# Kernel tuning notes

Measured on AMD Instinct MI355X. Metric: run time of the kernel, lower is better.

The kernel has to match this reference:

```python
import jax, jax.numpy as jnp
import numpy as np

N = 100000          # num nodes
E = 1_600_000       # num edges (avg degree 16)
IN = 512
OUT = 64
HOPS = 4


def setup_inputs() -> dict:
    key = jax.random.key(0)
    k1, k2, k3 = jax.random.split(key, 3)
    x = jax.random.normal(k1, (N, IN), dtype=jnp.float32)
    W = jax.random.normal(k2, (OUT, IN), dtype=jnp.float32) * 0.02
    b = jnp.zeros((OUT,), dtype=jnp.float32)
    edge_index = jax.random.randint(k3, (2, E), 0, N, dtype=jnp.int32)
    return {"x": x, "W": W, "b": b, "edge_index": edge_index}


def reference(x, W, b, edge_index):
    # 1) linear projection first (low-memory SGC variant)
    h = x @ W.T + b                      # [N, OUT]
    n = h.shape[0]

    # 2) gcn_norm: add self loops, symmetric D^{-1/2} A D^{-1/2}
    row, col = edge_index[0], edge_index[1]
    loop = jnp.arange(n, dtype=row.dtype)
    row = jnp.concatenate([row, loop])   # [E+N]
    col = jnp.concatenate([col, loop])
    ew = jnp.ones(row.shape[0], dtype=h.dtype)
    deg = jax.ops.segment_sum(ew, col, num_segments=n)          # in-degree incl. self loop
    dinv = jnp.where(deg > 0, jax.lax.rsqrt(deg), 0.0)
    w = dinv[row] * ew * dinv[col]       # normalized edge weights [E+N]

    # 3) hops x SpMM: adj_t built with (row=col, col=row) => out[col] += w * h[row]
    for _ in range(HOPS):
        h = jax.ops.segment_sum(w[:, None] * h[row], col, num_segments=n)
    return h
```

## Files before the change

### kernel.cpp

```cpp
#include <hip/hip_runtime.h>
#include <stdint.h>

#define IN_DIM 512
#define OUT_DIM 64

typedef short bf16x8 __attribute__((ext_vector_type(8)));
typedef float f32x4 __attribute__((ext_vector_type(4)));

__device__ inline unsigned short f2bf(float f) {
    unsigned int u = __float_as_uint(f);
    return (unsigned short)((u + 0x7FFFu + ((u >> 16) & 1u)) >> 16);
}
__device__ inline float bf2f(unsigned short s) {
    return __uint_as_float(((unsigned int)s) << 16);
}

__global__ void zero_deg_kernel(int* __restrict__ deg, int N) {
    int i = blockIdx.x * blockDim.x + threadIdx.x;
    if (i < N) deg[i] = 0;
}

__global__ __launch_bounds__(256) void hist_part_kernel(const int* __restrict__ col,
                                                        int* __restrict__ deg, int E, int N) {
    int part = blockIdx.x & 7;
    int lo = (int)((long)part * N / 8);
    int hi = (int)((long)(part + 1) * N / 8);
    int stride = (gridDim.x >> 3) * blockDim.x;
    int i = (blockIdx.x >> 3) * blockDim.x + threadIdx.x;
    for (; i < E; i += stride) {
        int c = col[i];
        if (c >= lo && c < hi) atomicAdd(&deg[c], 1);
    }
}

__global__ void dinv_kernel(const int* __restrict__ deg, float* __restrict__ dinv,
                            float* __restrict__ d2, int N) {
    int i = blockIdx.x * blockDim.x + threadIdx.x;
    if (i < N) {
        float d = (float)deg[i] + 1.0f;
        dinv[i] = 1.0f / sqrtf(d);
        d2[i] = 1.0f / d;
    }
}

__global__ void pack_w_kernel(const float* __restrict__ W,
                              unsigned short* __restrict__ Bhi,
                              unsigned short* __restrict__ Blo) {
    int tid = blockIdx.x * blockDim.x + threadIdx.x;
    if (tid >= 4096) return;
    int L = tid & 63;
    int ct = tid >> 6;
    int t = ct & 15, c = ct >> 4;
    int o = c * 16 + (L & 15);
    int k0 = t * 32 + (L >> 4) * 8;
    const float* src = W + (size_t)o * IN_DIM + k0;
    #pragma unroll
    for (int j = 0; j < 8; ++j) {
        float w = src[j];
        unsigned short h = f2bf(w);
        Bhi[(size_t)tid * 8 + j] = h;
        Blo[(size_t)tid * 8 + j] = f2bf(w - bf2f(h));
    }
}

__global__ __launch_bounds__(1024) void scan_local_kernel(const int* __restrict__ deg,
                                                          int* __restrict__ rowptr,
                                                          int* __restrict__ bsum, int N) {
    __shared__ int sm[16];
    int tid = threadIdx.x, lane = tid & 63, wid = tid >> 6;
    int i = blockIdx.x * 4096 + tid * 4;
    int4 v = make_int4(0, 0, 0, 0);
    if (i + 3 < N) {
        v = *(const int4*)(deg + i);
    } else {
        if (i < N) v.x = deg[i];
        if (i + 1 < N) v.y = deg[i + 1];
        if (i + 2 < N) v.z = deg[i + 2];
        if (i + 3 < N) v.w = deg[i + 3];
    }
    int s1 = v.x, s2 = s1 + v.y, s3 = s2 + v.z, s4 = s3 + v.w;
    int incl = s4;
    #pragma unroll
    for (int d = 1; d < 64; d <<= 1) {
        int t = __shfl_up(incl, d, 64);
        if (lane >= d) incl += t;
    }
    if (lane == 63) sm[wid] = incl;
    __syncthreads();
    if (tid == 0) {
        int run = 0;
        #pragma unroll
        for (int w2 = 0; w2 < 16; ++w2) { int t = sm[w2]; sm[w2] = run; run += t; }
        bsum[blockIdx.x] = run;
    }
    __syncthreads();
    int tbase = incl - s4 + sm[wid];
    if (i + 3 < N) {
        *(int4*)(rowptr + i) = make_int4(tbase, tbase + s1, tbase + s2, tbase + s3);
    } else {
        if (i < N)     rowptr[i]     = tbase;
        if (i + 1 < N) rowptr[i + 1] = tbase + s1;
        if (i + 2 < N) rowptr[i + 2] = tbase + s2;
        if (i + 3 < N) rowptr[i + 3] = tbase + s3;
    }
}

__global__ __launch_bounds__(1024) void scan_add_kernel(int* __restrict__ rowptr,
                                                        int* __restrict__ cursor,
                                                        const int* __restrict__ bsum,
                                                        int N, int nb) {
    __shared__ int soff;
    if (threadIdx.x == 0) {
        int off = 0;
        for (int j = 0; j < (int)blockIdx.x; ++j) off += bsum[j];
        soff = off;
        if ((int)blockIdx.x == nb - 1) {
            int tot = off;
            for (int j = blockIdx.x; j < nb; ++j) tot += bsum[j];
            rowptr[N] = tot;
        }
    }
    __syncthreads();
    int off = soff;
    int i = blockIdx.x * 4096 + threadIdx.x * 4;
    if (i + 3 < N) {
        int4 r = *(int4*)(rowptr + i);
        r.x += off; r.y += off; r.z += off; r.w += off;
        *(int4*)(rowptr + i) = r;
        *(int4*)(cursor + i) = r;
    } else {
        for (int j = 0; j < 4; ++j)
            if (i + j < N) { int r = rowptr[i + j] + off; rowptr[i + j] = r; cursor[i + j] = r; }
    }
}

__global__ __launch_bounds__(256) void fill_part_kernel(const int* __restrict__ row,
                                                        const int* __restrict__ col,
                                                        int* __restrict__ cursor,
                                                        int* __restrict__ csr, int E, int N) {
    int part = blockIdx.x & 7;
    int lo = (int)((long)part * N / 8);
    int hi = (int)((long)(part + 1) * N / 8);
    int stride = (gridDim.x >> 3) * blockDim.x;
    int i = (blockIdx.x >> 3) * blockDim.x + threadIdx.x;
    for (; i < E; i += stride) {
        int c = col[i];
        if (c >= lo && c < hi) {
            int pos = atomicAdd(&cursor[c], 1);
            csr[pos] = row[i];
        }
    }
}

__global__ __launch_bounds__(256) void mfma_gemm_kernel(const float* __restrict__ x,
                                                        const unsigned short* __restrict__ Bhi,
                                                        const unsigned short* __restrict__ Blo,
                                                        const float* __restrict__ bias,
                                                        const float* __restrict__ dinv,
                                                        float* __restrict__ h, int N) {
    int lane = threadIdx.x & 63;
    int wid  = __builtin_amdgcn_readfirstlane(threadIdx.x >> 6);
    int quad = lane >> 4, r16 = lane & 15;
    long rowBase = ((long)blockIdx.x * 4 + wid) * 32;
    if (rowBase >= N) return;
    bool full = (rowBase + 32 <= N);

    f32x4 acc[2][4];
    #pragma unroll
    for (int rt = 0; rt < 2; ++rt)
        #pragma unroll
        for (int c = 0; c < 4; ++c) acc[rt][c] = (f32x4){0.f, 0.f, 0.f, 0.f};

    int row0 = (int)rowBase + r16;
    int row1 = (int)rowBase + 16 + r16;
    int row0c = full ? row0 : (row0 < N ? row0 : N - 1);
    int row1c = full ? row1 : (row1 < N ? row1 : N - 1);
    const float* a0p = x + (size_t)row0c * IN_DIM + quad * 8;
    const float* a1p = x + (size_t)row1c * IN_DIM + quad * 8;

    for (int t = 0; t < 16; ++t) {
        bf16x8 bh[4], bl[4];
        #pragma unroll
        for (int c = 0; c < 4; ++c) {
            size_t off = ((size_t)(c * 16 + t) * 64 + lane) * 8;
            union { int4 i; bf16x8 b; } uh, ul;
            uh.i = *(const int4*)(Bhi + off);
            ul.i = *(const int4*)(Blo + off);
            bh[c] = uh.b; bl[c] = ul.b;
        }
        bf16x8 ah[2], al[2];
        #pragma unroll
        for (int rt = 0; rt < 2; ++rt) {
            const float* p = (rt ? a1p : a0p) + t * 32;
            float4 f0 = *(const float4*)p;
            float4 f1 = *(const float4*)(p + 4);
            float v[8] = {f0.x, f0.y, f0.z, f0.w, f1.x, f1.y, f1.z, f1.w};
            #pragma unroll
            for (int j = 0; j < 8; ++j) {
                unsigned short hi = f2bf(v[j]);
                ah[rt][j] = (short)hi;
                al[rt][j] = (short)f2bf(v[j] - bf2f(hi));
            }
        }
        #pragma unroll
        for (int rt = 0; rt < 2; ++rt)
            #pragma unroll
            for (int c = 0; c < 4; ++c) {
                acc[rt][c] = __builtin_amdgcn_mfma_f32_16x16x32_bf16(ah[rt], bh[c], acc[rt][c], 0, 0, 0);
                acc[rt][c] = __builtin_amdgcn_mfma_f32_16x16x32_bf16(ah[rt], bl[c], acc[rt][c], 0, 0, 0);
                acc[rt][c] = __builtin_amdgcn_mfma_f32_16x16x32_bf16(al[rt], bh[c], acc[rt][c], 0, 0, 0);
            }
    }

    float bb[4];
    #pragma unroll
    for (int c = 0; c < 4; ++c) bb[c] = bias[c * 16 + r16];
    #pragma unroll
    for (int rt = 0; rt < 2; ++rt)
        #pragma unroll
        for (int rr = 0; rr < 4; ++rr) {
            int row = (int)rowBase + rt * 16 + quad * 4 + rr;
            if (row < N) {
                float dv = dinv[row];
                #pragma unroll
                for (int c = 0; c < 4; ++c)
                    h[(size_t)row * OUT_DIM + c * 16 + r16] = dv * (acc[rt][c][rr] + bb[c]);
            }
        }
}

#define HOP_K 8

__global__ __launch_bounds__(256) void hop_kernel(const float* __restrict__ src,
                                                  float* __restrict__ dst,
                                                  const int* __restrict__ csr,
                                                  const int* __restrict__ rowptr,
                                                  const float* __restrict__ scale, int N) {
    int lane = threadIdx.x & 63;
    int wid  = __builtin_amdgcn_readfirstlane(threadIdx.x >> 6);
    int g    = lane >> 4;
    int l16  = lane & 15;
    int w  = blockIdx.x * 4 + wid;
    int n0 = w * HOP_K;
    if (n0 >= N) return;
    int nK = (N - n0 < HOP_K) ? (N - n0) : HOP_K;

    int rpv = 0;
    if (lane <= nK) rpv = rowptr[n0 + lane];

    for (int j = 0; j < nK; ++j) {
        int n = n0 + j;
        int s = __shfl(rpv, j, 64);
        int e = __shfl(rpv, j + 1, 64);

        f32x4 self4;
        if (lane < 16) self4 = *(const f32x4*)(src + (size_t)n * OUT_DIM + l16 * 4);

        f32x4 acc = (f32x4){0.f, 0.f, 0.f, 0.f};
        int i = s;
        for (; i + 16 <= e; i += 16) {
            int base = i + 4 * g;
            int i0 = csr[base], i1 = csr[base + 1], i2 = csr[base + 2], i3 = csr[base + 3];
            f32x4 v0 = *(const f32x4*)(src + (size_t)i0 * OUT_DIM + l16 * 4);
            f32x4 v1 = *(const f32x4*)(src + (size_t)i1 * OUT_DIM + l16 * 4);
            f32x4 v2 = *(const f32x4*)(src + (size_t)i2 * OUT_DIM + l16 * 4);
            f32x4 v3 = *(const f32x4*)(src + (size_t)i3 * OUT_DIM + l16 * 4);
            acc += (v0 + v1) + (v2 + v3);
        }
        for (; i + 4 <= e; i += 4) {
            int i0 = csr[i + g];
            acc += *(const f32x4*)(src + (size_t)i0 * OUT_DIM + l16 * 4);
        }
        if (i + g < e) {
            int i0 = csr[i + g];
            acc += *(const f32x4*)(src + (size_t)i0 * OUT_DIM + l16 * 4);
        }
        #pragma unroll
        for (int d = 16; d < 64; d <<= 1) {
            acc.x += __shfl_xor(acc.x, d, 64);
            acc.y += __shfl_xor(acc.y, d, 64);
            acc.z += __shfl_xor(acc.z, d, 64);
            acc.w += __shfl_xor(acc.w, d, 64);
        }
        if (lane < 16) {
            float sc = scale[n];
            f32x4 r = (acc + self4) * sc;
            *(f32x4*)(dst + (size_t)n * OUT_DIM + l16 * 4) = r;
        }
    }
}

extern "C" void kernel_launch(void* const* d_in, const int* in_sizes, int n_in,
                              void* d_out, int out_size, void* d_ws, size_t ws_size,
                              hipStream_t stream) {
    const float* x  = (const float*)d_in[0];
    const float* W  = (const float*)d_in[1];
    const float* b  = (const float*)d_in[2];
    const int*   ei = (const int*)d_in[3];
    int N = in_sizes[0] / IN_DIM;
    int E = in_sizes[3] / 2;
    const int* row = ei;
    const int* col = ei + E;
    float* out = (float*)d_out;

    float* dinv   = (float*)d_ws;
    float* d2     = dinv + N;
    int*   deg    = (int*)(d2 + N);
    int*   rowptr = deg + N;
    int*   cursor = rowptr + (N + 4);
    int*   bsum   = cursor + N;
    unsigned short* Bhi = (unsigned short*)(bsum + 32);
    unsigned short* Blo = Bhi + 32768;

    float* xspace = (float*)d_in[0];
    float* hbuf   = xspace;
    int*   csr    = (int*)(xspace + (size_t)N * OUT_DIM);

    dim3 blk(256);
    int gN = (N + 255) / 256;
    int gPart = 8 * 784;
    int nbScan = (N + 4095) / 4096;

    zero_deg_kernel<<<gN, blk, 0, stream>>>(deg, N);
    hist_part_kernel<<<gPart, blk, 0, stream>>>(col, deg, E, N);
    dinv_kernel<<<gN, blk, 0, stream>>>(deg, dinv, d2, N);

    pack_w_kernel<<<16, blk, 0, stream>>>(W, Bhi, Blo);

    mfma_gemm_kernel<<<(N + 127) / 128, blk, 0, stream>>>(x, Bhi, Blo, b, dinv, out, N);

    scan_local_kernel<<<nbScan, 1024, 0, stream>>>(deg, rowptr, bsum, N);
    scan_add_kernel<<<nbScan, 1024, 0, stream>>>(rowptr, cursor, bsum, N, nbScan);
    fill_part_kernel<<<gPart, blk, 0, stream>>>(row, col, cursor, csr, E, N);

    int chunks = (N + HOP_K - 1) / HOP_K;
    int gH = (chunks + 3) / 4;
    hop_kernel<<<gH, blk, 0, stream>>>(out, hbuf, csr, rowptr, d2, N);
    hop_kernel<<<gH, blk, 0, stream>>>(hbuf, out, csr, rowptr, d2, N);
    hop_kernel<<<gH, blk, 0, stream>>>(out, hbuf, csr, rowptr, d2, N);
    hop_kernel<<<gH, blk, 0, stream>>>(hbuf, out, csr, rowptr, dinv, N);
}
```

Measured before the change: 715.2 us.

## Partition hop features into 8-column slabs to shrink gather working set

```diff
diff --git a/kernel.cpp b/kernel.cpp
--- a/kernel.cpp
+++ b/kernel.cpp
@@ -223,8 +223,11 @@
             if (row < N) {
                 float dv = dinv[row];
                 #pragma unroll
-                for (int c = 0; c < 4; ++c)
-                    h[(size_t)row * OUT_DIM + c * 16 + r16] = dv * (acc[rt][c][rr] + bb[c]);
+                for (int c = 0; c < 4; ++c) {
+                    int colIdx = c * 16 + r16;
+                    h[((size_t)(colIdx >> 3) * N + row) * 8 + (colIdx & 7)] =
+                        dv * (acc[rt][c][rr] + bb[c]);
+                }
             }
         }
 }
@@ -235,15 +238,18 @@
                                                   float* __restrict__ dst,
                                                   const int* __restrict__ csr,
                                                   const int* __restrict__ rowptr,
-                                                  const float* __restrict__ scale, int N) {
+                                                  const float* __restrict__ scale,
+                                                  int N, int rowMajorOut) {
     int lane = threadIdx.x & 63;
     int wid  = __builtin_amdgcn_readfirstlane(threadIdx.x >> 6);
-    int g    = lane >> 4;
-    int l16  = lane & 15;
-    int w  = blockIdx.x * 4 + wid;
-    int n0 = w * HOP_K;
+    int p    = blockIdx.x & 7;
+    int el   = lane & 15;
+    int q    = lane >> 4;
+    int n0   = (blockIdx.x >> 3) * (4 * HOP_K) + wid * HOP_K;
     if (n0 >= N) return;
     int nK = (N - n0 < HOP_K) ? (N - n0) : HOP_K;
+
+    const float* cs = src + (size_t)p * N * 8;
 
     int rpv = 0;
     if (lane <= nK) rpv = rowptr[n0 + lane];
@@ -252,40 +258,43 @@
         int n = n0 + j;
         int s = __shfl(rpv, j, 64);
         int e = __shfl(rpv, j + 1, 64);
-
-        f32x4 self4;
-        if (lane < 16) self4 = *(const f32x4*)(src + (size_t)n * OUT_DIM + l16 * 4);
-
-        f32x4 acc = (f32x4){0.f, 0.f, 0.f, 0.f};
-        int i = s;
-        for (; i + 16 <= e; i += 16) {
-            int base = i + 4 * g;
-            int i0 = csr[base], i1 = csr[base + 1], i2 = csr[base + 2], i3 = csr[base + 3];
-            f32x4 v0 = *(const f32x4*)(src + (size_t)i0 * OUT_DIM + l16 * 4);
-            f32x4 v1 = *(const f32x4*)(src + (size_t)i1 * OUT_DIM + l16 * 4);
-            f32x4 v2 = *(const f32x4*)(src + (size_t)i2 * OUT_DIM + l16 * 4);
-            f32x4 v3 = *(const f32x4*)(src + (size_t)i3 * OUT_DIM + l16 * 4);
-            acc += (v0 + v1) + (v2 + v3);
-        }
-        for (; i + 4 <= e; i += 4) {
-            int i0 = csr[i + g];
-            acc += *(const f32x4*)(src + (size_t)i0 * OUT_DIM + l16 * 4);
-        }
-        if (i + g < e) {
-            int i0 = csr[i + g];
-            acc += *(const f32x4*)(src + (size_t)i0 * OUT_DIM + l16 * 4);
-        }
-        #pragma unroll
-        for (int d = 16; d < 64; d <<= 1) {
-            acc.x += __shfl_xor(acc.x, d, 64);
-            acc.y += __shfl_xor(acc.y, d, 64);
-            acc.z += __shfl_xor(acc.z, d, 64);
-            acc.w += __shfl_xor(acc.w, d, 64);
-        }
-        if (lane < 16) {
+        int d = e - s;
+
+        float ax = 0.f, ay = 0.f;
+        if (d > 0) {
+            int last = e - 1;
+            int a0 = s + el;       if (a0 > last) a0 = last;
+            int a1 = s + el + 16;  if (a1 > last) a1 = last;
+            int i0 = csr[a0];
+            int i1 = csr[a1];
+            float2 v0 = *(const float2*)(cs + (size_t)i0 * 8 + q * 2);
+            float2 v1 = *(const float2*)(cs + (size_t)i1 * 8 + q * 2);
+            if (el < d)      { ax += v0.x; ay += v0.y; }
+            if (el + 16 < d) { ax += v1.x; ay += v1.y; }
+            if (d > 32) {
+                for (int i = s + 32; i < e; i += 16) {
+                    int a = i + el; if (a > last) a = last;
+                    int ii = csr[a];
+                    float2 v = *(const float2*)(cs + (size_t)ii * 8 + q * 2);
+                    if (i + el < e) { ax += v.x; ay += v.y; }
+                }
+            }
+        }
+        #pragma unroll
+        for (int dd = 1; dd < 16; dd <<= 1) {
+            ax += __shfl_xor(ax, dd, 64);
+            ay += __shfl_xor(ay, dd, 64);
+        }
+        if (el == 0) {
+            float2 self = *(const float2*)(cs + (size_t)n * 8 + q * 2);
             float sc = scale[n];
-            f32x4 r = (acc + self4) * sc;
-            *(f32x4*)(dst + (size_t)n * OUT_DIM + l16 * 4) = r;
+            float2 r;
+            r.x = (ax + self.x) * sc;
+            r.y = (ay + self.y) * sc;
+            if (rowMajorOut)
+                *(float2*)(dst + (size_t)n * OUT_DIM + p * 8 + q * 2) = r;
+            else
+                *(float2*)(dst + ((size_t)p * N + n) * 8 + q * 2) = r;
         }
     }
 }
@@ -333,10 +342,10 @@
     scan_add_kernel<<<nbScan, 1024, 0, stream>>>(rowptr, cursor, bsum, N, nbScan);
     fill_part_kernel<<<gPart, blk, 0, stream>>>(row, col, cursor, csr, E, N);
 
-    int chunks = (N + HOP_K - 1) / HOP_K;
-    int gH = (chunks + 3) / 4;
-    hop_kernel<<<gH, blk, 0, stream>>>(out, hbuf, csr, rowptr, d2, N);
-    hop_kernel<<<gH, blk, 0, stream>>>(hbuf, out, csr, rowptr, d2, N);
-    hop_kernel<<<gH, blk, 0, stream>>>(out, hbuf, csr, rowptr, d2, N);
-    hop_kernel<<<gH, blk, 0, stream>>>(hbuf, out, csr, rowptr, dinv, N);
-}
+    int bpc = (N + 4 * HOP_K - 1) / (4 * HOP_K);
+    int gH = bpc * 8;
+    hop_kernel<<<gH, blk, 0, stream>>>(out, hbuf, csr, rowptr, d2, N, 0);
+    hop_kernel<<<gH, blk, 0, stream>>>(hbuf, out, csr, rowptr, d2, N, 0);
+    hop_kernel<<<gH, blk, 0, stream>>>(out, hbuf, csr, rowptr, d2, N, 0);
+    hop_kernel<<<gH, blk, 0, stream>>>(hbuf, out, csr, rowptr, dinv, N, 1);
+}
```

Result: slower. 1.200 ms (+67.8%).
